# Optimization experiments

Hardware: AMD Instinct MI355X
Metric: run time of the kernel (lower is better)

The kernel has to match this reference:

```python
import jax, jax.numpy as jnp
import numpy as np

EMBED = 768
HEADS = 8
HEAD_DIM = EMBED // HEADS  # 96


def setup_inputs() -> dict:
    key = jax.random.key(0)
    k1, k2, k3, k4, k5 = jax.random.split(key, 5)
    b, n = 4, 2048
    x = jax.random.normal(k1, (b, n, EMBED), dtype=jnp.float32)
    s = 1.0 / np.sqrt(EMBED)
    W_qkv = jax.random.normal(k2, (EMBED, 3 * EMBED), dtype=jnp.float32) * s
    b_qkv = jax.random.normal(k3, (3 * EMBED,), dtype=jnp.float32) * 0.02
    W_proj = jax.random.normal(k4, (EMBED, EMBED), dtype=jnp.float32) * s
    b_proj = jax.random.normal(k5, (EMBED,), dtype=jnp.float32) * 0.02
    return {"x": x, "W_qkv": W_qkv, "b_qkv": b_qkv, "W_proj": W_proj, "b_proj": b_proj}


def reference(x, W_qkv, b_qkv, W_proj, b_proj):
    b, n, _ = x.shape
    qkv = x @ W_qkv + b_qkv  # [b, n, 3*EMBED]
    # rearrange 'b n (h d qkv) -> qkv b h n d': qkv is fastest-varying axis
    qkv = qkv.reshape(b, n, HEADS, HEAD_DIM, 3)
    q = jnp.transpose(qkv[..., 0], (0, 2, 1, 3))  # [b, h, n, d]
    k = jnp.transpose(qkv[..., 1], (0, 2, 1, 3))
    v = jnp.transpose(qkv[..., 2], (0, 2, 1, 3))
    scale = 1.0 / np.sqrt(HEAD_DIM)
    energy = jnp.einsum('bhqd,bhkd->bhqk', q, k) * scale
    attn = jax.nn.softmax(energy, axis=-1)  # dropout p=0 -> identity
    out = jnp.einsum('bhqk,bhkd->bhqd', attn, v)
    out = jnp.transpose(out, (0, 2, 1, 3)).reshape(b, n, EMBED)
    out = out @ W_proj + b_proj
    return out
```

## Files before the change

kernel.cpp:

```cpp
#include <hip/hip_runtime.h>
#include <hip/hip_bf16.h>

#define EMBED 768
#define NHEADS 8
#define HDIM 96
#define SEQ 2048
#define BATCH 4
#define NTOK (BATCH*SEQ)
#define QKVN (3*EMBED)

#define QSCALE 0.14724444f

typedef __attribute__((ext_vector_type(4))) float f32x4;
typedef __attribute__((ext_vector_type(16))) float f32x16;
typedef __attribute__((ext_vector_type(8))) __bf16 bf16x8;

__device__ __forceinline__ unsigned short f2bf(float f) {
  union { float f; unsigned int u; } c; c.f = f;
  unsigned int u = c.u;
  return (unsigned short)((u + 0x7FFFu + ((u >> 16) & 1u)) >> 16);
}

__device__ __forceinline__ unsigned int cvt_pk_bf16(float lo, float hi) {
  unsigned int r;
  asm("v_cvt_pk_bf16_f32 %0, %1, %2" : "=v"(r) : "v"(lo), "v"(hi));
  return r;
}

__device__ __forceinline__ void gload_lds16(const void* g, void* l) {
  __builtin_amdgcn_global_load_lds(
      (const __attribute__((address_space(1))) unsigned int*)g,
      (__attribute__((address_space(3))) unsigned int*)l, 16, 0, 0);
}

__global__ __launch_bounds__(256) void cast_x_kernel(const float4* __restrict__ in,
                                                     ushort4* __restrict__ out, int n4) {
  int i = blockIdx.x * 256 + threadIdx.x;
  if (i >= n4) return;
  float4 v = in[i];
  out[i] = make_ushort4(f2bf(v.x), f2bf(v.y), f2bf(v.z), f2bf(v.w));
}

__global__ __launch_bounds__(256) void transpose_cast_kernel(const float* __restrict__ in,
                                                             unsigned short* __restrict__ out,
                                                             int R, int C, int remap) {
  __shared__ float t[32][33];
  int c0 = blockIdx.x * 32, r0 = blockIdx.y * 32;
  int tx = threadIdx.x & 31, ty = threadIdx.x >> 5;
  #pragma unroll
  for (int i = 0; i < 32; i += 8)
    t[ty + i][tx] = in[(size_t)(r0 + ty + i) * C + c0 + tx];
  __syncthreads();
  #pragma unroll
  for (int i = 0; i < 32; i += 8) {
    int c = c0 + ty + i;
    int rp = remap ? (c % 3) * 768 + c / 3 : c;
    out[(size_t)rp * R + r0 + tx] = f2bf(t[tx][ty + i]);
  }
}

template <int MODE>
__global__ __launch_bounds__(256, 2) void gemm8_kernel(
    const unsigned short* __restrict__ A, const unsigned short* __restrict__ B,
    const float* __restrict__ bias, int K, int NB,
    unsigned short* __restrict__ Qo, unsigned short* __restrict__ Ko,
    unsigned short* __restrict__ Vt, float* __restrict__ out) {
  __shared__ unsigned short As[2][128 * 64];
  __shared__ unsigned short Bs[2][128 * 64];
  const int tid = threadIdx.x;
  const int lane = tid & 63, wid = tid >> 6;
  const int wr = wid >> 1, wc = wid & 1;
  const int l15 = lane & 15, l16 = lane >> 4;
  const int cpx = gridDim.x >> 3;
  const int bid = blockIdx.x;
  const int swz = (bid & 7) * cpx + (bid >> 3);
  const int my = swz / NB, nx = swz - my * NB;
  const int m0 = my * 128, n0 = nx * 128;

  auto stage_half = [&](int buf, int kt, int half) {
    const unsigned short* src = half ? B : A;
    const int base0 = half ? n0 : m0;
    char* dst = (char*)(half ? &Bs[buf][0] : &As[buf][0]);
    #pragma unroll
    for (int i = 0; i < 4; i++) {
      int c = i * 256 + tid;
      int r = c >> 3, s = c & 7;
      gload_lds16(src + (size_t)(base0 + r) * K + kt * 64 + ((s ^ (r & 7)) << 3),
                  dst + (i * 256 + wid * 64) * 16);
    }
  };

  f32x4 acc[4][4] = {};
  const int xr = (l15 & 7) << 4;

  stage_half(0, 0, 0);
  stage_half(0, 0, 1);
  asm volatile("s_waitcnt vmcnt(0)" ::: "memory");
  __builtin_amdgcn_s_barrier();

  const int NT = K >> 6;
  for (int t = 0; t < NT; ++t) {
    const int cur = t & 1;
    const char* Ac = (const char*)&As[cur][0];
    const char* Bc = (const char*)&Bs[cur][0];
    #pragma unroll
    for (int kh = 0; kh < 2; ++kh) {
      bf16x8 af[4], bfr[4];
      #pragma unroll
      for (int mi = 0; mi < 4; mi++)
        af[mi] = *(const bf16x8*)(Ac + (wr * 64 + mi * 16 + l15) * 128 +
                                  ((kh * 64 + l16 * 16) ^ xr));
      #pragma unroll
      for (int ni = 0; ni < 4; ni++)
        bfr[ni] = *(const bf16x8*)(Bc + (wc * 64 + ni * 16 + l15) * 128 +
                                   ((kh * 64 + l16 * 16) ^ xr));
      if (t + 1 < NT) stage_half(cur ^ 1, t + 1, kh);
      __builtin_amdgcn_s_barrier();
      __builtin_amdgcn_s_setprio(1);
      #pragma unroll
      for (int mi = 0; mi < 4; mi++)
        #pragma unroll
        for (int ni = 0; ni < 4; ni++)
          acc[mi][ni] = __builtin_amdgcn_mfma_f32_16x16x32_bf16(af[mi], bfr[ni], acc[mi][ni], 0, 0, 0);
      __builtin_amdgcn_s_setprio(0);
      __builtin_amdgcn_s_barrier();
    }
    asm volatile("s_waitcnt lgkmcnt(0)" ::: "memory");
    asm volatile("s_waitcnt vmcnt(0)" ::: "memory");
    __builtin_amdgcn_sched_barrier(0);
    __builtin_amdgcn_s_barrier();
  }

  if (MODE == 0) {
    #pragma unroll
    for (int mi = 0; mi < 4; mi++) {
      #pragma unroll
      for (int ni = 0; ni < 4; ni++) {
        int base = n0 + wc * 64 + ni * 16;
        int which = base / 768;
        int hd = base - which * 768;
        int h = hd / 96;
        int d0 = hd - h * 96;
        float bb = bias[(hd + l15) * 3 + which];
        int rowb = m0 + wr * 64 + mi * 16 + l16 * 4;
        int bi = rowb >> 11, nnb = rowb & 2047;
        size_t bh = (size_t)(bi * NHEADS + h);
        if (which == 2) {
          int nn2 = (nnb & ~12) | ((nnb & 4) << 1) | ((nnb & 8) >> 1);
          float v0 = acc[mi][ni][0] + bb, v1 = acc[mi][ni][1] + bb;
          float v2 = acc[mi][ni][2] + bb, v3 = acc[mi][ni][3] + bb;
          uint2 pk;
          pk.x = cvt_pk_bf16(v0, v1);
          pk.y = cvt_pk_bf16(v2, v3);
          *(uint2*)(Vt + (bh * HDIM + d0 + l15) * SEQ + nn2) = pk;
        } else {
          #pragma unroll
          for (int j = 0; j < 4; j++) {
            float v = acc[mi][ni][j] + bb;
            int nn = nnb + j;
            if (which == 0) Qo[(bh * SEQ + nn) * HDIM + d0 + l15] = f2bf(v * QSCALE);
            else            Ko[(bh * SEQ + nn) * HDIM + d0 + l15] = f2bf(v);
          }
        }
      }
    }
  } else {
    #pragma unroll
    for (int mi = 0; mi < 4; mi++) {
      #pragma unroll
      for (int ni = 0; ni < 4; ni++) {
        int col = n0 + wc * 64 + ni * 16 + l15;
        float bb = bias[col];
        #pragma unroll
        for (int j = 0; j < 4; j++) {
          int row = m0 + wr * 64 + mi * 16 + l16 * 4 + j;
          out[(size_t)row * EMBED + col] = acc[mi][ni][j] + bb;
        }
      }
    }
  }
}

__global__ __launch_bounds__(256) void attn_kernel(
    const unsigned short* __restrict__ Q, const unsigned short* __restrict__ Kd,
    const unsigned short* __restrict__ Vt, unsigned short* __restrict__ Oa) {
  __shared__ unsigned short Ks[2][64 * 96];
  __shared__ unsigned short Vs[2][96 * 64];

  const int tid = threadIdx.x, lane = tid & 63, wid = tid >> 6;
  const int l31 = lane & 31, hi = lane >> 5;
  const int bid = blockIdx.x;
  const int swz = (bid & 7) * 64 + (bid >> 3);
  const int qb_ = swz & 15, bh = swz >> 4;
  const int bi = bh >> 3, h = bh & 7;
  const int q0 = qb_ * 128;

  const unsigned short* Qg = Q + ((size_t)bh * SEQ + q0) * HDIM;
  const unsigned short* Kg = Kd + (size_t)bh * SEQ * HDIM;
  const unsigned short* Vg = Vt + (size_t)bh * HDIM * SEQ;

  bf16x8 qf[6];
  #pragma unroll
  for (int ks = 0; ks < 6; ks++)
    qf[ks] = *(const bf16x8*)(Qg + (size_t)(wid * 32 + l31) * HDIM + ks * 16 + hi * 8);

  auto stageKV = [&](int buf, int k0) {
    #pragma unroll
    for (int i = 0; i < 3; i++) {
      int g = i * 256 + tid;
      int o = g >> 6, kv = g & 63;
      gload_lds16(Kg + (size_t)(k0 + kv) * HDIM + o * 8,
                  (char*)&Ks[buf][0] + (i * 256 + wid * 64) * 16);
    }
    #pragma unroll
    for (int i = 0; i < 3; i++) {
      int idx = i * 256 + tid;
      int d = idx >> 3, s = idx & 7;
      gload_lds16(Vg + (size_t)d * SEQ + k0 + ((s ^ (d & 7)) << 3),
                  (char*)&Vs[buf][0] + (i * 256 + wid * 64) * 16);
    }
  };

  f32x16 oacc[3] = {};
  float mrow = -__builtin_inff(), lrow = 0.f;

  stageKV(0, 0);
  __syncthreads();

  for (int kb = 0; kb < SEQ / 64; kb++) {
    const int cur = kb & 1;
    if (kb + 1 < SEQ / 64) stageKV(cur ^ 1, (kb + 1) * 64);

    const char* Kc = (const char*)&Ks[cur][0];
    const char* Vc = (const char*)&Vs[cur][0];

    f32x16 sacc[2] = {};
    #pragma unroll
    for (int ks = 0; ks < 6; ks++) {
      bf16x8 ak0 = *(const bf16x8*)(Kc + (((2 * ks + hi) * 64) + l31) * 16);
      bf16x8 ak1 = *(const bf16x8*)(Kc + (((2 * ks + hi) * 64) + 32 + l31) * 16);
      __builtin_amdgcn_s_setprio(1);
      sacc[0] = __builtin_amdgcn_mfma_f32_32x32x16_bf16(ak0, qf[ks], sacc[0], 0, 0, 0);
      sacc[1] = __builtin_amdgcn_mfma_f32_32x32x16_bf16(ak1, qf[ks], sacc[1], 0, 0, 0);
      __builtin_amdgcn_s_setprio(0);
    }

    bf16x8 vball[4][3];
    #pragma unroll
    for (int s = 0; s < 4; s++) {
      const int sidx = s * 2 + hi;
      #pragma unroll
      for (int db = 0; db < 3; db++) {
        int d = db * 32 + l31;
        vball[s][db] = *(const bf16x8*)(Vc + d * 128 + ((sidx ^ (d & 7)) << 4));
      }
    }

    float v = fmaxf(sacc[0][0], sacc[1][0]);
    #pragma unroll
    for (int r = 1; r < 16; r++)
      v = fmaxf(v, fmaxf(sacc[0][r], sacc[1][r]));
    v = fmaxf(v, __shfl_xor(v, 32));
    if (!__all(v - mrow <= 11.54f)) {
      float mnew = fmaxf(mrow, v);
      float alpha = __builtin_amdgcn_exp2f(mrow - mnew);
      mrow = mnew;
      lrow *= alpha;
      #pragma unroll
      for (int db = 0; db < 3; db++)
        #pragma unroll
        for (int r = 0; r < 16; r++)
          oacc[db][r] *= alpha;
    }

    unsigned int pk[2][8];
    float psum = 0.f;
    #pragma unroll
    for (int kbk = 0; kbk < 2; kbk++)
      #pragma unroll
      for (int j2 = 0; j2 < 8; j2++) {
        float p0 = __builtin_amdgcn_exp2f(sacc[kbk][2 * j2] - mrow);
        float p1 = __builtin_amdgcn_exp2f(sacc[kbk][2 * j2 + 1] - mrow);
        psum += p0 + p1;
        pk[kbk][j2] = cvt_pk_bf16(p0, p1);
      }
    psum += __shfl_xor(psum, 32);
    lrow += psum;

    #pragma unroll
    for (int kbk = 0; kbk < 2; kbk++)
      #pragma unroll
      for (int tt = 0; tt < 2; tt++) {
        union { unsigned int u[4]; bf16x8 v; } pf;
        pf.u[0] = pk[kbk][4 * tt];     pf.u[1] = pk[kbk][4 * tt + 1];
        pf.u[2] = pk[kbk][4 * tt + 2]; pf.u[3] = pk[kbk][4 * tt + 3];
        __builtin_amdgcn_s_setprio(1);
        #pragma unroll
        for (int db = 0; db < 3; db++)
          oacc[db] = __builtin_amdgcn_mfma_f32_32x32x16_bf16(vball[kbk * 2 + tt][db], pf.v, oacc[db], 0, 0, 0);
        __builtin_amdgcn_s_setprio(0);
      }

    __syncthreads();
  }

  {
    const float rl = 1.f / lrow;
    const int tok = q0 + wid * 32 + l31;
    unsigned short* Og = Oa + ((size_t)bi * SEQ + tok) * EMBED + h * HDIM;
    #pragma unroll
    for (int db = 0; db < 3; db++)
      #pragma unroll
      for (int rq = 0; rq < 4; rq++) {
        uint2 o;
        o.x = cvt_pk_bf16(oacc[db][4 * rq] * rl, oacc[db][4 * rq + 1] * rl);
        o.y = cvt_pk_bf16(oacc[db][4 * rq + 2] * rl, oacc[db][4 * rq + 3] * rl);
        *(uint2*)(Og + db * 32 + rq * 8 + hi * 4) = o;
      }
  }
}

extern "C" void kernel_launch(void* const* d_in, const int* in_sizes, int n_in,
                              void* d_out, int out_size, void* d_ws, size_t ws_size,
                              hipStream_t stream) {
  const float* x      = (const float*)d_in[0];
  const float* W_qkv  = (const float*)d_in[1];
  const float* b_qkv  = (const float*)d_in[2];
  const float* W_proj = (const float*)d_in[3];
  const float* b_proj = (const float*)d_in[4];
  float* out = (float*)d_out;

  char* ws = (char*)d_ws;
  size_t off = 0;
  auto alloc = [&](size_t bytes) { void* p = ws + off; off += (bytes + 255) & ~(size_t)255; return p; };
  unsigned short* xb  = (unsigned short*)alloc((size_t)NTOK * EMBED * 2);
  unsigned short* WqT = (unsigned short*)alloc((size_t)QKVN * EMBED * 2);
  unsigned short* WpT = (unsigned short*)alloc((size_t)EMBED * EMBED * 2);
  unsigned short* Qb  = (unsigned short*)alloc((size_t)NTOK * EMBED * 2);
  unsigned short* Kb  = (unsigned short*)alloc((size_t)NTOK * EMBED * 2);
  unsigned short* Vtb = (unsigned short*)alloc((size_t)NTOK * EMBED * 2);
  unsigned short* Ob  = (unsigned short*)alloc((size_t)NTOK * EMBED * 2);

  cast_x_kernel<<<dim3(NTOK * EMBED / 4 / 256), dim3(256), 0, stream>>>(
      (const float4*)x, (ushort4*)xb, NTOK * EMBED / 4);
  transpose_cast_kernel<<<dim3(QKVN / 32, EMBED / 32), dim3(256), 0, stream>>>(W_qkv, WqT, EMBED, QKVN, 1);
  transpose_cast_kernel<<<dim3(EMBED / 32, EMBED / 32), dim3(256), 0, stream>>>(W_proj, WpT, EMBED, EMBED, 0);

  gemm8_kernel<0><<<dim3((NTOK / 128) * (QKVN / 128)), dim3(256), 0, stream>>>(
      xb, WqT, b_qkv, EMBED, QKVN / 128, Qb, Kb, Vtb, nullptr);

  attn_kernel<<<dim3(BATCH * NHEADS * (SEQ / 128)), dim3(256), 0, stream>>>(Qb, Kb, Vtb, Ob);

  gemm8_kernel<1><<<dim3((NTOK / 128) * (EMBED / 128)), dim3(256), 0, stream>>>(
      Ob, WpT, b_proj, EMBED, EMBED / 128, nullptr, nullptr, nullptr, out);
}
```

Baseline: 159.5 us.

## Software-pipeline PV MFMA of previous KV tile behind current tile's softmax

```diff
diff --git a/kernel.cpp b/kernel.cpp
--- a/kernel.cpp
+++ b/kernel.cpp
@@ -223,43 +223,52 @@
 
   f32x16 oacc[3] = {};
   float mrow = -__builtin_inff(), lrow = 0.f;
+  unsigned int pk[2][8];
+  bf16x8 vball[4][3];
 
   stageKV(0, 0);
   __syncthreads();
 
-  for (int kb = 0; kb < SEQ / 64; kb++) {
+  const int NT = SEQ / 64;
+  for (int kb = 0; kb < NT; kb++) {
     const int cur = kb & 1;
-    if (kb + 1 < SEQ / 64) stageKV(cur ^ 1, (kb + 1) * 64);
+    if (kb + 1 < NT) stageKV(cur ^ 1, (kb + 1) * 64);
 
     const char* Kc = (const char*)&Ks[cur][0];
     const char* Vc = (const char*)&Vs[cur][0];
 
-    f32x16 sacc[2] = {};
+    f32x16 ns0 = {}, ns1 = {};
     #pragma unroll
     for (int ks = 0; ks < 6; ks++) {
       bf16x8 ak0 = *(const bf16x8*)(Kc + (((2 * ks + hi) * 64) + l31) * 16);
       bf16x8 ak1 = *(const bf16x8*)(Kc + (((2 * ks + hi) * 64) + 32 + l31) * 16);
       __builtin_amdgcn_s_setprio(1);
-      sacc[0] = __builtin_amdgcn_mfma_f32_32x32x16_bf16(ak0, qf[ks], sacc[0], 0, 0, 0);
-      sacc[1] = __builtin_amdgcn_mfma_f32_32x32x16_bf16(ak1, qf[ks], sacc[1], 0, 0, 0);
+      ns0 = __builtin_amdgcn_mfma_f32_32x32x16_bf16(ak0, qf[ks], ns0, 0, 0, 0);
+      ns1 = __builtin_amdgcn_mfma_f32_32x32x16_bf16(ak1, qf[ks], ns1, 0, 0, 0);
       __builtin_amdgcn_s_setprio(0);
     }
 
-    bf16x8 vball[4][3];
-    #pragma unroll
-    for (int s = 0; s < 4; s++) {
-      const int sidx = s * 2 + hi;
-      #pragma unroll
-      for (int db = 0; db < 3; db++) {
-        int d = db * 32 + l31;
-        vball[s][db] = *(const bf16x8*)(Vc + d * 128 + ((sidx ^ (d & 7)) << 4));
-      }
-    }
-
-    float v = fmaxf(sacc[0][0], sacc[1][0]);
+    if (kb) {
+      #pragma unroll
+      for (int kbk = 0; kbk < 2; kbk++)
+        #pragma unroll
+        for (int tt = 0; tt < 2; tt++) {
+          union { unsigned int u[4]; bf16x8 v; } pf;
+          pf.u[0] = pk[kbk][4 * tt];     pf.u[1] = pk[kbk][4 * tt + 1];
+          pf.u[2] = pk[kbk][4 * tt + 2]; pf.u[3] = pk[kbk][4 * tt + 3];
+          __builtin_amdgcn_s_setprio(1);
+          #pragma unroll
+          for (int db = 0; db < 3; db++)
+            oacc[db] = __builtin_amdgcn_mfma_f32_32x32x16_bf16(
+                vball[kbk * 2 + tt][db], pf.v, oacc[db], 0, 0, 0);
+          __builtin_amdgcn_s_setprio(0);
+        }
+    }
+
+    float v = fmaxf(ns0[0], ns1[0]);
     #pragma unroll
     for (int r = 1; r < 16; r++)
-      v = fmaxf(v, fmaxf(sacc[0][r], sacc[1][r]));
+      v = fmaxf(v, fmaxf(ns0[r], ns1[r]));
     v = fmaxf(v, __shfl_xor(v, 32));
     if (!__all(v - mrow <= 11.54f)) {
       float mnew = fmaxf(mrow, v);
@@ -272,37 +281,49 @@
         for (int r = 0; r < 16; r++)
           oacc[db][r] *= alpha;
     }
-
-    unsigned int pk[2][8];
     float psum = 0.f;
     #pragma unroll
-    for (int kbk = 0; kbk < 2; kbk++)
-      #pragma unroll
-      for (int j2 = 0; j2 < 8; j2++) {
-        float p0 = __builtin_amdgcn_exp2f(sacc[kbk][2 * j2] - mrow);
-        float p1 = __builtin_amdgcn_exp2f(sacc[kbk][2 * j2 + 1] - mrow);
-        psum += p0 + p1;
-        pk[kbk][j2] = cvt_pk_bf16(p0, p1);
-      }
+    for (int j2 = 0; j2 < 8; j2++) {
+      float p0 = __builtin_amdgcn_exp2f(ns0[2 * j2] - mrow);
+      float p1 = __builtin_amdgcn_exp2f(ns0[2 * j2 + 1] - mrow);
+      psum += p0 + p1;
+      pk[0][j2] = cvt_pk_bf16(p0, p1);
+    }
+    #pragma unroll
+    for (int j2 = 0; j2 < 8; j2++) {
+      float p0 = __builtin_amdgcn_exp2f(ns1[2 * j2] - mrow);
+      float p1 = __builtin_amdgcn_exp2f(ns1[2 * j2 + 1] - mrow);
+      psum += p0 + p1;
+      pk[1][j2] = cvt_pk_bf16(p0, p1);
+    }
     psum += __shfl_xor(psum, 32);
     lrow += psum;
 
     #pragma unroll
-    for (int kbk = 0; kbk < 2; kbk++)
-      #pragma unroll
-      for (int tt = 0; tt < 2; tt++) {
-        union { unsigned int u[4]; bf16x8 v; } pf;
-        pf.u[0] = pk[kbk][4 * tt];     pf.u[1] = pk[kbk][4 * tt + 1];
-        pf.u[2] = pk[kbk][4 * tt + 2]; pf.u[3] = pk[kbk][4 * tt + 3];
-        __builtin_amdgcn_s_setprio(1);
-        #pragma unroll
-        for (int db = 0; db < 3; db++)
-          oacc[db] = __builtin_amdgcn_mfma_f32_32x32x16_bf16(vball[kbk * 2 + tt][db], pf.v, oacc[db], 0, 0, 0);
-        __builtin_amdgcn_s_setprio(0);
+    for (int s = 0; s < 4; s++) {
+      const int sidx = s * 2 + hi;
+      #pragma unroll
+      for (int db = 0; db < 3; db++) {
+        int d = db * 32 + l31;
+        vball[s][db] = *(const bf16x8*)(Vc + d * 128 + ((sidx ^ (d & 7)) << 4));
       }
+    }
 
     __syncthreads();
   }
+
+  #pragma unroll
+  for (int kbk = 0; kbk < 2; kbk++)
+    #pragma unroll
+    for (int tt = 0; tt < 2; tt++) {
+      union { unsigned int u[4]; bf16x8 v; } pf;
+      pf.u[0] = pk[kbk][4 * tt];     pf.u[1] = pk[kbk][4 * tt + 1];
+      pf.u[2] = pk[kbk][4 * tt + 2]; pf.u[3] = pk[kbk][4 * tt + 3];
+      #pragma unroll
+      for (int db = 0; db < 3; db++)
+        oacc[db] = __builtin_amdgcn_mfma_f32_32x32x16_bf16(
+            vball[kbk * 2 + tt][db], pf.v, oacc[db], 0, 0, 0);
+    }
 
   {
     const float rl = 1.f / lrow;
```

Result: no change. 162.5 us (+1.9%).
